# Performance work log

Measured on AMD Instinct MI355X. Metric: run time of the kernel, lower is better.

## Reference

```python
import jax, jax.numpy as jnp
import numpy as np

FEAT_STRIDE = 16
SCALES = np.array([8.0, 16.0, 32.0], np.float32)
RATIOS = np.array([0.5, 1.0, 2.0], np.float32)
PRE_NMS = 6000
POST_NMS = 300
NMS_THRESH = 0.7
MIN_SIZE = 16.0


def _base_anchors():
    bs = float(FEAT_STRIDE)
    ctr = (bs - 1.0) * 0.5
    size = bs * bs
    ws = np.round(np.sqrt(size / RATIOS))
    hs = np.round(ws * RATIOS)
    anchors = []
    for w, h in zip(ws, hs):
        for s in SCALES:
            ww, hh = w * s, h * s
            anchors.append([ctr - 0.5 * (ww - 1), ctr - 0.5 * (hh - 1),
                            ctr + 0.5 * (ww - 1), ctr + 0.5 * (hh - 1)])
    return np.array(anchors, np.float32)  # [A=9, 4]


def _all_anchors(H, W):
    base = _base_anchors()
    sx = np.arange(W, dtype=np.float32) * FEAT_STRIDE
    sy = np.arange(H, dtype=np.float32) * FEAT_STRIDE
    gx, gy = np.meshgrid(sx, sy)  # [H, W]
    shifts = np.stack([gx.ravel(), gy.ravel(), gx.ravel(), gy.ravel()], axis=1)  # [H*W, 4]
    return jnp.asarray((shifts[:, None, :] + base[None, :, :]).reshape(-1, 4))  # [H*W*A, 4]


def _conv2d(x, w, b, pad):
    y = jax.lax.conv_general_dilated(x, w, (1, 1), pad,
                                     dimension_numbers=('NCHW', 'OIHW', 'NCHW'))
    return y + b[None, :, None, None]


def _decode(anchors, deltas):
    wa = anchors[:, 2] - anchors[:, 0] + 1.0
    ha = anchors[:, 3] - anchors[:, 1] + 1.0
    cxa = anchors[:, 0] + 0.5 * wa
    cya = anchors[:, 1] + 0.5 * ha
    cx = deltas[:, 0] * wa + cxa
    cy = deltas[:, 1] * ha + cya
    w = wa * jnp.exp(deltas[:, 2])
    h = ha * jnp.exp(deltas[:, 3])
    return jnp.stack([cx - 0.5 * w, cy - 0.5 * h, cx + 0.5 * w, cy + 0.5 * h], axis=1)


def _pairwise_iou(b):
    x1, y1, x2, y2 = b[:, 0], b[:, 1], b[:, 2], b[:, 3]
    areas = (x2 - x1 + 1.0) * (y2 - y1 + 1.0)
    iw = jnp.clip(jnp.minimum(x2[:, None], x2[None, :]) - jnp.maximum(x1[:, None], x1[None, :]) + 1.0, 0.0)
    ih = jnp.clip(jnp.minimum(y2[:, None], y2[None, :]) - jnp.maximum(y1[:, None], y1[None, :]) + 1.0, 0.0)
    inter = iw * ih
    return inter / (areas[:, None] + areas[None, :] - inter)


def _proposal(bbox_pred, scores, anchors, im_info):
    boxes = _decode(anchors, bbox_pred)
    x1 = jnp.clip(boxes[:, 0], 0.0, im_info[1] - 1.0)
    y1 = jnp.clip(boxes[:, 1], 0.0, im_info[0] - 1.0)
    x2 = jnp.clip(boxes[:, 2], 0.0, im_info[1] - 1.0)
    y2 = jnp.clip(boxes[:, 3], 0.0, im_info[0] - 1.0)
    boxes = jnp.stack([x1, y1, x2, y2], axis=1)
    min_sz = MIN_SIZE * im_info[2]
    valid = ((x2 - x1 + 1.0) >= min_sz) & ((y2 - y1 + 1.0) >= min_sz)
    sc = jnp.where(valid, scores, -1.0)
    top_sc, idx = jax.lax.top_k(sc, PRE_NMS)
    props = boxes[idx]  # [PRE_NMS, 4], score-descending
    iou = _pairwise_iou(props)

    def body(i, keep):
        sup = (iou[i] > NMS_THRESH) & keep[i]
        return keep & ~(sup & (jnp.arange(PRE_NMS) > i))

    keep = jax.lax.fori_loop(0, PRE_NMS, body, jnp.ones((PRE_NMS,), bool))
    keep = keep & (top_sc > 0.0)
    order = jnp.argsort(jnp.logical_not(keep), stable=True)  # kept first, score order preserved
    sel = order[:POST_NMS]
    mask = (jnp.arange(POST_NMS) < jnp.sum(keep))[:, None]
    return jnp.where(mask, props[sel], 0.0)


def setup_inputs() -> dict:
    key = jax.random.key(0)
    ks = jax.random.split(key, 4)
    feature_map = jax.random.normal(ks[0], (1, 1024, 84, 125), jnp.float32)
    im_info = jnp.array([1344.0, 2000.0, 1.0], jnp.float32)  # (H, W, scale)
    conv_w = jax.random.normal(ks[1], (512, 1024, 3, 3), jnp.float32) * 0.01
    conv_b = jnp.zeros((512,), jnp.float32)
    cls_w = jax.random.normal(ks[2], (18, 512, 1, 1), jnp.float32) * 0.01
    cls_b = jnp.zeros((18,), jnp.float32)
    reg_w = jax.random.normal(ks[3], (36, 512, 1, 1), jnp.float32) * 0.01
    reg_b = jnp.zeros((36,), jnp.float32)
    return {"feature_map": feature_map, "im_info": im_info, "conv_w": conv_w,
            "conv_b": conv_b, "cls_w": cls_w, "cls_b": cls_b, "reg_w": reg_w, "reg_b": reg_b}


def reference(feature_map, im_info, conv_w, conv_b, cls_w, cls_b, reg_w, reg_b):
    B, C, H, W = feature_map.shape
    anchors = _all_anchors(H, W)  # [H*W*9, 4]
    fm = jax.nn.relu(_conv2d(feature_map, conv_w, conv_b, [(1, 1), (1, 1)]))
    cls = _conv2d(fm, cls_w, cls_b, [(0, 0), (0, 0)])  # [B, 18, H, W]
    reg = _conv2d(fm, reg_w, reg_b, [(0, 0), (0, 0)])  # [B, 36, H, W]
    cls_scores = cls.transpose(0, 2, 3, 1).reshape(-1, 2)
    bbox_pred = reg.transpose(0, 2, 3, 1).reshape(-1, 4)
    fg_probs = jax.nn.softmax(jax.lax.stop_gradient(cls_scores), axis=1)[:, 1]
    rois = _proposal(bbox_pred, fg_probs, anchors, im_info)
    return (bbox_pred, cls_scores, rois, anchors)
```

## Files before the change

kernel.cpp:

```cpp
#include <hip/hip_runtime.h>

typedef unsigned int u32;
typedef unsigned long long u64;

#define H_ 84
#define W_ 125
#define CIN 1024
#define CMID 512
#define NPOS 10500
#define NA 94500
#define PRE 6000
#define POST 300
#define FMROW 128
#define FMSTRIDE 10752
#define SELCAP 16384

__constant__ float c_aw[9] = {184.f, 368.f, 736.f, 128.f, 256.f, 512.f, 88.f, 176.f, 352.f};
__constant__ float c_ah[9] = { 96.f, 192.f, 384.f, 128.f, 256.f, 512.f, 176.f, 352.f, 704.f};

#define OFF_FM      0ull
#define OFF_BOXES   22020096ull
#define OFF_KEYS    23532096ull
#define OFF_SELA    24288096ull
#define OFF_SELB    24419168ull
#define OFF_PROPS   24550240ull
#define OFF_AREAS   24646240ull
#define OFF_VALIDW  24670240ull
#define OFF_MASK    24671008ull
#define OFF_KEEPW   29279008ull

__global__ __launch_bounds__(256, 4) void k_conv3(const float* __restrict__ in,
                                                  const float* __restrict__ w,
                                                  const float* __restrict__ bias,
                                                  float* __restrict__ fm) {
  __shared__ float Xs[16 * 4 * 132];
  const int tid = threadIdx.x;
  const int lane = tid & 63;
  const int wvi = __builtin_amdgcn_readfirstlane(tid >> 6);
  const int ocb = blockIdx.x;
  const int y0 = blockIdx.y * 2;
  const int oc0 = ocb * 16 + wvi * 4;

  float acc[4][2][2];
#pragma unroll
  for (int o = 0; o < 4; ++o)
#pragma unroll
    for (int r = 0; r < 2; ++r) {
      acc[o][r][0] = 0.f;
      acc[o][r][1] = 0.f;
    }

  const int cb = 2 * lane;

  float rbuf[33];
#pragma unroll
  for (int k = 0; k < 33; ++k) {
    const int l = tid + k * 256;
    const int r132 = l / 132;
    const int c = l - r132 * 132;
    const int i = r132 >> 2;
    const int rr = r132 & 3;
    const int yi = y0 - 1 + rr;
    const int xi = c - 1;
    float v = 0.f;
    if ((unsigned)yi < 84u && (unsigned)xi < 125u)
      v = in[i * (H_ * W_) + yi * W_ + xi];
    rbuf[k] = v;
  }

#pragma unroll 1
  for (int icb = 0; icb < CIN; icb += 16) {
    __syncthreads();
#pragma unroll
    for (int k = 0; k < 33; ++k) Xs[tid + k * 256] = rbuf[k];
    __syncthreads();

    const int icb2 = (icb + 16 < CIN) ? icb + 16 : icb;
#pragma unroll
    for (int k = 0; k < 33; ++k) {
      const int l = tid + k * 256;
      const int r132 = l / 132;
      const int c = l - r132 * 132;
      const int i = r132 >> 2;
      const int rr = r132 & 3;
      const int yi = y0 - 1 + rr;
      const int xi = c - 1;
      float v = 0.f;
      if ((unsigned)yi < 84u && (unsigned)xi < 125u)
        v = in[(icb2 + i) * (H_ * W_) + yi * W_ + xi];
      rbuf[k] = v;
    }

#pragma unroll 2
    for (int i = 0; i < 16; ++i) {
      const int ic = icb + i;
      float ws[4][9];
#pragma unroll
      for (int o = 0; o < 4; ++o)
#pragma unroll
        for (int e = 0; e < 9; ++e)
          ws[o][e] = w[(oc0 + o) * 9216 + ic * 9 + e];

      float x4[4][4];
#pragma unroll
      for (int rr = 0; rr < 4; ++rr) {
        float2 lo = *(const float2*)&Xs[(i * 4 + rr) * 132 + cb];
        float2 hi = *(const float2*)&Xs[(i * 4 + rr) * 132 + cb + 2];
        x4[rr][0] = lo.x;
        x4[rr][1] = lo.y;
        x4[rr][2] = hi.x;
        x4[rr][3] = hi.y;
      }

#pragma unroll
      for (int o = 0; o < 4; ++o)
#pragma unroll
        for (int r = 0; r < 2; ++r)
#pragma unroll
          for (int ky = 0; ky < 3; ++ky)
#pragma unroll
            for (int kx = 0; kx < 3; ++kx) {
              float wv2 = ws[o][ky * 3 + kx];
              acc[o][r][0] += wv2 * x4[r + ky][kx];
              acc[o][r][1] += wv2 * x4[r + ky][kx + 1];
            }
    }
  }

  const int px = 2 * lane;
#pragma unroll
  for (int o = 0; o < 4; ++o) {
    float b = bias[oc0 + o];
#pragma unroll
    for (int r = 0; r < 2; ++r) {
      float2 v;
      v.x = fmaxf(acc[o][r][0] + b, 0.f);
      v.y = fmaxf(acc[o][r][1] + b, 0.f);
      *(float2*)&fm[(oc0 + o) * FMSTRIDE + (y0 + r) * FMROW + px] = v;
    }
  }
}

__global__ __launch_bounds__(64) void k_heads(const float* __restrict__ fm,
                                              const float* __restrict__ cls_w,
                                              const float* __restrict__ cls_b,
                                              const float* __restrict__ reg_w,
                                              const float* __restrict__ reg_b,
                                              const float* __restrict__ iminfo,
                                              float* __restrict__ out_bbox,
                                              float* __restrict__ out_cls,
                                              float* __restrict__ out_anch,
                                              float* __restrict__ boxes,
                                              uint2* __restrict__ keys) {
  __shared__ float wl[64 * 56];
  const int tid = threadIdx.x;
  const int p = blockIdx.x * 64 + tid;
  const int pc = p < NPOS ? p : NPOS - 1;
  const int py = pc / W_;
  const int px = pc % W_;
  const int pos = py * FMROW + px;

  float acc[56];
#pragma unroll
  for (int o = 0; o < 56; ++o) acc[o] = 0.f;

#pragma unroll 1
  for (int icb = 0; icb < CMID; icb += 64) {
    __syncthreads();
    for (int l = tid; l < 64 * 54; l += 64) {
      int ic = l / 54;
      int o = l % 54;
      float wv = (o < 18) ? cls_w[o * CMID + icb + ic] : reg_w[(o - 18) * CMID + icb + ic];
      wl[ic * 56 + o] = wv;
    }
    __syncthreads();
#pragma unroll 4
    for (int i = 0; i < 64; ++i) {
      float v = fm[(icb + i) * FMSTRIDE + pos];
#pragma unroll
      for (int o4 = 0; o4 < 14; ++o4) {
        float4 w4 = *(const float4*)&wl[i * 56 + o4 * 4];
        acc[o4 * 4 + 0] += w4.x * v;
        acc[o4 * 4 + 1] += w4.y * v;
        acc[o4 * 4 + 2] += w4.z * v;
        acc[o4 * 4 + 3] += w4.w * v;
      }
    }
  }
  if (p >= NPOS) return;

  const float imh = iminfo[0];
  const float imw = iminfo[1];
  const float minsz = 16.0f * iminfo[2];

#pragma unroll
  for (int a = 0; a < 9; ++a) {
    const int n = p * 9 + a;
    float s0 = acc[a * 2 + 0] + cls_b[a * 2 + 0];
    float s1 = acc[a * 2 + 1] + cls_b[a * 2 + 1];
    out_cls[n * 2 + 0] = s0;
    out_cls[n * 2 + 1] = s1;

    float dx = acc[18 + a * 4 + 0] + reg_b[a * 4 + 0];
    float dy = acc[18 + a * 4 + 1] + reg_b[a * 4 + 1];
    float dw = acc[18 + a * 4 + 2] + reg_b[a * 4 + 2];
    float dh = acc[18 + a * 4 + 3] + reg_b[a * 4 + 3];
    out_bbox[n * 4 + 0] = dx;
    out_bbox[n * 4 + 1] = dy;
    out_bbox[n * 4 + 2] = dw;
    out_bbox[n * 4 + 3] = dh;

    float aw = c_aw[a], ah = c_ah[a];
    float cxs = px * 16.0f + 7.5f;
    float cys = py * 16.0f + 7.5f;
    float ax1 = cxs - 0.5f * (aw - 1.0f);
    float ay1 = cys - 0.5f * (ah - 1.0f);
    float ax2 = cxs + 0.5f * (aw - 1.0f);
    float ay2 = cys + 0.5f * (ah - 1.0f);
    out_anch[n * 4 + 0] = ax1;
    out_anch[n * 4 + 1] = ay1;
    out_anch[n * 4 + 2] = ax2;
    out_anch[n * 4 + 3] = ay2;

    float wa = ax2 - ax1 + 1.0f;
    float ha = ay2 - ay1 + 1.0f;
    float cxa = ax1 + 0.5f * wa;
    float cya = ay1 + 0.5f * ha;
    float cx = dx * wa + cxa;
    float cy = dy * ha + cya;
    float ww = wa * expf(dw);
    float hh = ha * expf(dh);
    float bx1 = cx - 0.5f * ww;
    float by1 = cy - 0.5f * hh;
    float bx2 = cx + 0.5f * ww;
    float by2 = cy + 0.5f * hh;
    bx1 = fminf(fmaxf(bx1, 0.f), imw - 1.f);
    by1 = fminf(fmaxf(by1, 0.f), imh - 1.f);
    bx2 = fminf(fmaxf(bx2, 0.f), imw - 1.f);
    by2 = fminf(fmaxf(by2, 0.f), imh - 1.f);
    boxes[n * 4 + 0] = bx1;
    boxes[n * 4 + 1] = by1;
    boxes[n * 4 + 2] = bx2;
    boxes[n * 4 + 3] = by2;

    bool valid = (bx2 - bx1 + 1.0f >= minsz) && (by2 - by1 + 1.0f >= minsz);
    float prob = 1.0f / (1.0f + expf(s0 - s1));
    u32 key = valid ? __float_as_uint(prob) : 0u;
    keys[n] = make_uint2(~key, (u32)n);
  }
}

__global__ __launch_bounds__(512) void k_select(const uint2* __restrict__ keys,
                                                uint2* __restrict__ selA,
                                                uint2* __restrict__ selB) {
  __shared__ u32 h[8192];
  __shared__ u32 stot[512];
  __shared__ u32 sB1, sLt1, sB2, sN;
  const int t = threadIdx.x;
  const int s = t * 185;
  const int e = (s + 185 < NA) ? s + 185 : NA;

  for (int i = t; i < 4096; i += 512) h[i] = 0;
  __syncthreads();
  for (int i = s; i < e; ++i) atomicAdd(&h[keys[i].x >> 20], 1u);
  __syncthreads();
  {
    u32 loc = 0;
#pragma unroll
    for (int j = 0; j < 8; ++j) loc += h[t * 8 + j];
    stot[t] = loc;
    __syncthreads();
    for (int off = 1; off < 512; off <<= 1) {
      u32 add = (t >= off) ? stot[t - off] : 0u;
      __syncthreads();
      stot[t] += add;
      __syncthreads();
    }
    u32 cb = stot[t] - loc;
    if (cb < PRE && stot[t] >= PRE) {
      u32 run = cb;
#pragma unroll
      for (int j = 0; j < 8; ++j) {
        u32 c = h[t * 8 + j];
        if (run < PRE && run + c >= PRE) { sB1 = t * 8 + j; sLt1 = run; }
        run += c;
      }
    }
  }
  __syncthreads();
  const u32 B1 = sB1;
  const u32 T2 = PRE - sLt1;

  for (int i = t; i < 4096; i += 512) h[i] = 0;
  __syncthreads();
  for (int i = s; i < e; ++i) {
    u32 k = keys[i].x;
    if ((k >> 20) == B1) atomicAdd(&h[(k >> 8) & 0xFFFu], 1u);
  }
  __syncthreads();
  {
    u32 loc = 0;
#pragma unroll
    for (int j = 0; j < 8; ++j) loc += h[t * 8 + j];
    stot[t] = loc;
    __syncthreads();
    for (int off = 1; off < 512; off <<= 1) {
      u32 add = (t >= off) ? stot[t - off] : 0u;
      __syncthreads();
      stot[t] += add;
      __syncthreads();
    }
    u32 cb = stot[t] - loc;
    if (cb < T2 && stot[t] >= T2) {
      u32 run = cb;
#pragma unroll
      for (int j = 0; j < 8; ++j) {
        u32 c = h[t * 8 + j];
        if (run < T2 && run + c >= T2) { sB2 = t * 8 + j; }
        run += c;
      }
    }
  }
  __syncthreads();
  const u32 B2 = sB2;

  u32 cnt = 0;
  for (int i = s; i < e; ++i) {
    u32 k = keys[i].x;
    u32 hi = k >> 20;
    if (hi < B1 || (hi == B1 && ((k >> 8) & 0xFFFu) <= B2)) cnt++;
  }
  stot[t] = cnt;
  __syncthreads();
  for (int off = 1; off < 512; off <<= 1) {
    u32 add = (t >= off) ? stot[t - off] : 0u;
    __syncthreads();
    stot[t] += add;
    __syncthreads();
  }
  u32 base = stot[t] - cnt;
  if (t == 511) sN = stot[511] < SELCAP ? stot[511] : SELCAP;
  for (int i = s; i < e; ++i) {
    uint2 v = keys[i];
    u32 hi = v.x >> 20;
    if (hi < B1 || (hi == B1 && ((v.x >> 8) & 0xFFFu) <= B2)) {
      if (base < SELCAP) selA[base] = v;
      base++;
    }
  }
  __syncthreads();
  const int n = (int)sN;

  const int q = (n + 511) / 512;
  const int s2 = t * q;
  const int e2 = (s2 + q < n) ? s2 + q : n;
  uint2* src = selA;
  uint2* dst = selB;
#pragma unroll 1
  for (int pass = 0; pass < 8; ++pass) {
    const int sh = pass * 4;
#pragma unroll
    for (int k = 0; k < 16; ++k) h[k * 512 + t] = 0;
    __syncthreads();
    for (int i = s2; i < e2; ++i) {
      u32 d = (src[i].x >> sh) & 15u;
      h[d * 512 + t] += 1;
    }
    __syncthreads();
    u32 run = 0;
#pragma unroll
    for (int j = 0; j < 16; ++j) {
      u32 v = h[t * 16 + j];
      h[t * 16 + j] = run;
      run += v;
    }
    stot[t] = run;
    __syncthreads();
    for (int off = 1; off < 512; off <<= 1) {
      u32 add = (t >= off) ? stot[t - off] : 0u;
      __syncthreads();
      stot[t] += add;
      __syncthreads();
    }
    u32 cb = (t > 0) ? stot[t - 1] : 0u;
#pragma unroll
    for (int j = 0; j < 16; ++j) h[t * 16 + j] += cb;
    __syncthreads();
    for (int i = s2; i < e2; ++i) {
      uint2 v = src[i];
      u32 d = (v.x >> sh) & 15u;
      u32 off = h[d * 512 + t];
      h[d * 512 + t] = off + 1;
      dst[off] = v;
    }
    __syncthreads();
    uint2* tmp = src;
    src = dst;
    dst = tmp;
  }
}

__global__ __launch_bounds__(256) void k_gather(const uint2* __restrict__ sel,
                                                const float4* __restrict__ boxes,
                                                float4* __restrict__ props,
                                                float* __restrict__ areas,
                                                u64* __restrict__ validw) {
  const int k = blockIdx.x * 256 + threadIdx.x;
  bool valid = false;
  if (k < PRE) {
    uint2 kv = sel[k];
    u32 key = ~kv.x;
    valid = key > 0u;
    float4 b = boxes[kv.y];
    props[k] = b;
    areas[k] = (b.z - b.x + 1.0f) * (b.w - b.y + 1.0f);
  }
  u64 bal = __ballot(valid);
  if ((threadIdx.x & 63) == 0 && k < PRE) validw[k >> 6] = bal;
}

__global__ __launch_bounds__(256) void k_iou(const float4* __restrict__ props,
                                             const float* __restrict__ areas,
                                             u64* __restrict__ mask) {
  __shared__ float4 pj[64];
  __shared__ float aj[64];
  const int t = threadIdx.x;
  const int jw = blockIdx.x;
  const int i = blockIdx.y * 256 + t;
  if (t < 64) {
    const int jj = jw * 64 + t;
    float4 z = {0.f, 0.f, 0.f, 0.f};
    pj[t] = (jj < PRE) ? props[jj] : z;
    aj[t] = (jj < PRE) ? areas[jj] : 0.f;
  }
  __syncthreads();
  if (i >= PRE) return;
  const int j0 = jw * 64;
  u64 bits = 0;
  if (j0 + 63 > i) {
    const float4 bi = props[i];
    const float ai = areas[i];
#pragma unroll 8
    for (int b = 0; b < 64; ++b) {
      const int j = j0 + b;
      if (j > i && j < PRE) {
        float4 bj = pj[b];
        float iw = fminf(bi.z, bj.z) - fmaxf(bi.x, bj.x) + 1.0f;
        float ih = fminf(bi.w, bj.w) - fmaxf(bi.y, bj.y) + 1.0f;
        iw = fmaxf(iw, 0.f);
        ih = fmaxf(ih, 0.f);
        float inter = iw * ih;
        if (inter > 0.7f * (ai + aj[b] - inter)) bits |= (1ull << b);
      }
    }
  }
  mask[(u64)i * 96 + jw] = bits;
}

__device__ __forceinline__ u64 bcast_u64(u64 v, int src) {
  u32 lo = (u32)v;
  u32 hi = (u32)(v >> 32);
  lo = (u32)__shfl((int)lo, src, 64);
  hi = (u32)__shfl((int)hi, src, 64);
  return ((u64)hi << 32) | (u64)lo;
}

__global__ __launch_bounds__(64) void k_nms(const u64* __restrict__ mask,
                                            const u64* __restrict__ validw,
                                            u64* __restrict__ keepw) {
  const int lane = threadIdx.x;
  const int w0 = (2 * lane < 96) ? 2 * lane : 0;
  const int w1 = (2 * lane < 96) ? 2 * lane + 1 : 1;
  u64 s0 = 0, s1 = 0;
  u64 b0[16], b1[16];
#pragma unroll
  for (int d = 0; d < 16; ++d) {
    b0[d] = mask[(u64)d * 96 + w0];
    b1[d] = mask[(u64)d * 96 + w1];
  }
#pragma unroll 1
  for (int i0 = 0; i0 < PRE; i0 += 16) {
#pragma unroll
    for (int d = 0; d < 16; ++d) {
      int i = i0 + d;
      int w = i >> 6;
      u64 cand = (w & 1) ? s1 : s0;
      u64 word = bcast_u64(cand, w >> 1);
      bool sup = (word >> (i & 63)) & 1ull;
      if (!sup) {
        s0 |= b0[d];
        s1 |= b1[d];
      }
      int ip = i + 16;
      if (ip > PRE - 1) ip = PRE - 1;
      b0[d] = mask[(u64)ip * 96 + w0];
      b1[d] = mask[(u64)ip * 96 + w1];
    }
  }
  if (2 * lane < 94) keepw[2 * lane] = ~s0 & validw[2 * lane];
  if (2 * lane + 1 < 94) keepw[2 * lane + 1] = ~s1 & validw[2 * lane + 1];
}

__global__ __launch_bounds__(128) void k_emit(const u64* __restrict__ keepw,
                                              const float4* __restrict__ props,
                                              float* __restrict__ rois) {
  __shared__ u32 base[94];
  const int t = threadIdx.x;
  for (int r = t; r < POST * 4; r += 128) rois[r] = 0.f;
  if (t < 94) base[t] = (u32)__popcll(keepw[t]);
  __syncthreads();
  if (t == 0) {
    u32 run = 0;
    for (int q = 0; q < 94; ++q) {
      u32 c = base[q];
      base[q] = run;
      run += c;
    }
  }
  __syncthreads();
  if (t < 94) {
    u64 kw = keepw[t];
    int rank = (int)base[t];
    while (kw) {
      int b = __ffsll((unsigned long long)kw) - 1;
      kw &= kw - 1;
      if (rank < POST) {
        float4 v = props[t * 64 + b];
        rois[rank * 4 + 0] = v.x;
        rois[rank * 4 + 1] = v.y;
        rois[rank * 4 + 2] = v.z;
        rois[rank * 4 + 3] = v.w;
      }
      rank++;
    }
  }
}

extern "C" void kernel_launch(void* const* d_in, const int* in_sizes, int n_in,
                              void* d_out, int out_size, void* d_ws, size_t ws_size,
                              hipStream_t stream) {
  const float* feat   = (const float*)d_in[0];
  const float* iminfo = (const float*)d_in[1];
  const float* conv_w = (const float*)d_in[2];
  const float* conv_b = (const float*)d_in[3];
  const float* cls_w  = (const float*)d_in[4];
  const float* cls_b  = (const float*)d_in[5];
  const float* reg_w  = (const float*)d_in[6];
  const float* reg_b  = (const float*)d_in[7];

  float* out = (float*)d_out;
  float* out_bbox = out;
  float* out_cls  = out + 378000;
  float* out_rois = out + 567000;
  float* out_anch = out + 568200;

  char* ws = (char*)d_ws;
  float* fm      = (float*)(ws + OFF_FM);
  float* boxes   = (float*)(ws + OFF_BOXES);
  uint2* keysA   = (uint2*)(ws + OFF_KEYS);
  uint2* selA    = (uint2*)(ws + OFF_SELA);
  uint2* selB    = (uint2*)(ws + OFF_SELB);
  float4* props  = (float4*)(ws + OFF_PROPS);
  float* areas   = (float*)(ws + OFF_AREAS);
  u64* validw    = (u64*)(ws + OFF_VALIDW);
  u64* mask      = (u64*)(ws + OFF_MASK);
  u64* keepw     = (u64*)(ws + OFF_KEEPW);

  k_conv3<<<dim3(32, 42), 256, 0, stream>>>(feat, conv_w, conv_b, fm);
  k_heads<<<165, 64, 0, stream>>>(fm, cls_w, cls_b, reg_w, reg_b, iminfo,
                                  out_bbox, out_cls, out_anch, boxes, keysA);
  k_select<<<1, 512, 0, stream>>>(keysA, selA, selB);
  k_gather<<<24, 256, 0, stream>>>(selA, (const float4*)boxes, props, areas, validw);
  k_iou<<<dim3(94, 24), 256, 0, stream>>>(props, areas, mask);
  k_nms<<<1, 64, 0, stream>>>(mask, validw, keepw);
  k_emit<<<1, 128, 0, stream>>>(keepw, props, out_rois);
}
```

Measured before the change: 3.261 ms.

## Double-buffer conv3 input tiles, swizzle block order, aggregate histogram atomics

The 3x3 conv kernel now uses two shared-memory buffers of 8 input channels each and precomputes gather offsets with a validity bitmask. This removes the per-iteration address arithmetic and one of the two barriers per step, and halves the register prefetch buffer. The launch becomes 1D with a swizzle that groups blocks sharing output rows, aiming for better L2 reuse of input rows. The select kernel's histogram passes now use wave-level ballot aggregation, so each distinct bin gets one shared atomic per wave instead of one per thread, at the cost of extra ballot and shuffle loops.

```diff
diff --git a/kernel.cpp b/kernel.cpp
--- a/kernel.cpp
+++ b/kernel.cpp
@@ -33,12 +33,14 @@
                                                   const float* __restrict__ w,
                                                   const float* __restrict__ bias,
                                                   float* __restrict__ fm) {
-  __shared__ float Xs[16 * 4 * 132];
+  __shared__ float Xs[2][8 * 4 * 132];
   const int tid = threadIdx.x;
   const int lane = tid & 63;
   const int wvi = __builtin_amdgcn_readfirstlane(tid >> 6);
-  const int ocb = blockIdx.x;
-  const int y0 = blockIdx.y * 2;
+  const int bid = blockIdx.x;
+  const int swz = (bid & 7) * 168 + (bid >> 3);
+  const int ocb = swz & 31;
+  const int y0 = (swz >> 5) * 2;
   const int oc0 = ocb * 16 + wvi * 4;
 
   float acc[4][2][2];
@@ -52,9 +54,10 @@
 
   const int cb = 2 * lane;
 
-  float rbuf[33];
-#pragma unroll
-  for (int k = 0; k < 33; ++k) {
+  u32 offk[17];
+  u32 vmask = 0;
+#pragma unroll
+  for (int k = 0; k < 17; ++k) {
     const int l = tid + k * 256;
     const int r132 = l / 132;
     const int c = l - r132 * 132;
@@ -62,37 +65,33 @@
     const int rr = r132 & 3;
     const int yi = y0 - 1 + rr;
     const int xi = c - 1;
-    float v = 0.f;
-    if ((unsigned)yi < 84u && (unsigned)xi < 125u)
-      v = in[i * (H_ * W_) + yi * W_ + xi];
-    rbuf[k] = v;
-  }
+    const bool ok = (l < 4224) && ((unsigned)yi < 84u) && ((unsigned)xi < 125u);
+    offk[k] = ok ? (u32)(i * (H_ * W_) + yi * W_ + xi) : 0u;
+    if (ok) vmask |= (1u << k);
+  }
+
+  float rb[17];
+#pragma unroll
+  for (int k = 0; k < 17; ++k) rb[k] = (vmask >> k & 1) ? in[offk[k]] : 0.f;
+#pragma unroll
+  for (int k = 0; k < 17; ++k) {
+    const int l = tid + k * 256;
+    if (l < 4224) Xs[0][l] = rb[k];
+  }
+  __syncthreads();
 
 #pragma unroll 1
-  for (int icb = 0; icb < CIN; icb += 16) {
-    __syncthreads();
-#pragma unroll
-    for (int k = 0; k < 33; ++k) Xs[tid + k * 256] = rbuf[k];
-    __syncthreads();
-
-    const int icb2 = (icb + 16 < CIN) ? icb + 16 : icb;
-#pragma unroll
-    for (int k = 0; k < 33; ++k) {
-      const int l = tid + k * 256;
-      const int r132 = l / 132;
-      const int c = l - r132 * 132;
-      const int i = r132 >> 2;
-      const int rr = r132 & 3;
-      const int yi = y0 - 1 + rr;
-      const int xi = c - 1;
-      float v = 0.f;
-      if ((unsigned)yi < 84u && (unsigned)xi < 125u)
-        v = in[(icb2 + i) * (H_ * W_) + yi * W_ + xi];
-      rbuf[k] = v;
-    }
-
+  for (int t = 0; t < 128; ++t) {
+    const int cur = t & 1;
+    const int icn = (t + 1 < 128) ? (t + 1) * 8 : t * 8;
+    const u32 gbase = (u32)icn * (u32)(H_ * W_);
+#pragma unroll
+    for (int k = 0; k < 17; ++k)
+      rb[k] = (vmask >> k & 1) ? in[gbase + offk[k]] : 0.f;
+
+    const int icb = t * 8;
 #pragma unroll 2
-    for (int i = 0; i < 16; ++i) {
+    for (int i = 0; i < 8; ++i) {
       const int ic = icb + i;
       float ws[4][9];
 #pragma unroll
@@ -104,8 +103,8 @@
       float x4[4][4];
 #pragma unroll
       for (int rr = 0; rr < 4; ++rr) {
-        float2 lo = *(const float2*)&Xs[(i * 4 + rr) * 132 + cb];
-        float2 hi = *(const float2*)&Xs[(i * 4 + rr) * 132 + cb + 2];
+        float2 lo = *(const float2*)&Xs[cur][(i * 4 + rr) * 132 + cb];
+        float2 hi = *(const float2*)&Xs[cur][(i * 4 + rr) * 132 + cb + 2];
         x4[rr][0] = lo.x;
         x4[rr][1] = lo.y;
         x4[rr][2] = hi.x;
@@ -120,17 +119,24 @@
           for (int ky = 0; ky < 3; ++ky)
 #pragma unroll
             for (int kx = 0; kx < 3; ++kx) {
-              float wv2 = ws[o][ky * 3 + kx];
+              const float wv2 = ws[o][ky * 3 + kx];
               acc[o][r][0] += wv2 * x4[r + ky][kx];
               acc[o][r][1] += wv2 * x4[r + ky][kx + 1];
             }
     }
+
+#pragma unroll
+    for (int k = 0; k < 17; ++k) {
+      const int l = tid + k * 256;
+      if (l < 4224) Xs[cur ^ 1][l] = rb[k];
+    }
+    __syncthreads();
   }
 
   const int px = 2 * lane;
 #pragma unroll
   for (int o = 0; o < 4; ++o) {
-    float b = bias[oc0 + o];
+    const float b = bias[oc0 + o];
 #pragma unroll
     for (int r = 0; r < 2; ++r) {
       float2 v;
@@ -257,12 +263,25 @@
   __shared__ u32 stot[512];
   __shared__ u32 sB1, sLt1, sB2, sN;
   const int t = threadIdx.x;
+  const int lane = t & 63;
   const int s = t * 185;
   const int e = (s + 185 < NA) ? s + 185 : NA;
 
   for (int i = t; i < 4096; i += 512) h[i] = 0;
   __syncthreads();
-  for (int i = s; i < e; ++i) atomicAdd(&h[keys[i].x >> 20], 1u);
+  for (int k0 = 0; k0 < 185; ++k0) {
+    const int i = s + k0;
+    bool act = i < e;
+    u32 bin = act ? (keys[i].x >> 20) : 0u;
+    while (__any(act)) {
+      u64 am = __ballot(act);
+      int leader = (int)(__ffsll((unsigned long long)am) - 1);
+      u32 lb = (u32)__shfl((int)bin, leader, 64);
+      u64 same = __ballot(act && bin == lb);
+      if (lane == leader) atomicAdd(&h[lb], (u32)__popcll(same));
+      if (act && bin == lb) act = false;
+    }
+  }
   __syncthreads();
   {
     u32 loc = 0;
@@ -293,9 +312,19 @@
 
   for (int i = t; i < 4096; i += 512) h[i] = 0;
   __syncthreads();
-  for (int i = s; i < e; ++i) {
-    u32 k = keys[i].x;
-    if ((k >> 20) == B1) atomicAdd(&h[(k >> 8) & 0xFFFu], 1u);
+  for (int k0 = 0; k0 < 185; ++k0) {
+    const int i = s + k0;
+    u32 kx = (i < e) ? keys[i].x : 0u;
+    bool act = (i < e) && ((kx >> 20) == B1);
+    u32 bin = (kx >> 8) & 0xFFFu;
+    while (__any(act)) {
+      u64 am = __ballot(act);
+      int leader = (int)(__ffsll((unsigned long long)am) - 1);
+      u32 lb = (u32)__shfl((int)bin, leader, 64);
+      u64 same = __ballot(act && bin == lb);
+      if (lane == leader && same) atomicAdd(&h[lb], (u32)__popcll(same));
+      if (act && bin == lb) act = false;
+    }
   }
   __syncthreads();
   {
@@ -566,7 +595,7 @@
   u64* mask      = (u64*)(ws + OFF_MASK);
   u64* keepw     = (u64*)(ws + OFF_KEEPW);
 
-  k_conv3<<<dim3(32, 42), 256, 0, stream>>>(feat, conv_w, conv_b, fm);
+  k_conv3<<<1344, 256, 0, stream>>>(feat, conv_w, conv_b, fm);
   k_heads<<<165, 64, 0, stream>>>(fm, cls_w, cls_b, reg_w, reg_b, iminfo,
                                   out_bbox, out_cls, out_anch, boxes, keysA);
   k_select<<<1, 512, 0, stream>>>(keysA, selA, selB);
```

New measurement: 3.380 ms. 1.04x slower.

## Use packed FP32 FMA in conv3x3 and remap blocks across XCDs

Applied to the files above, without the earlier changes.

Rewrites the 3x3 conv inner loop to use v_pk_fma_f32 through inline asm, with weights packed into scalar register pairs, so each instruction does two FMAs. It also flattens the grid to 1D and remaps block ids so each XCD works on a contiguous group of output-channel blocks, aiming for better L2 reuse of weights. The input prefetch now precomputes offsets and a validity mask once instead of recomputing index math every iteration. The risks are inline asm constraints (an SGPR operand needs uniform weights) and higher register pressure.

```diff
diff --git a/kernel.cpp b/kernel.cpp
--- a/kernel.cpp
+++ b/kernel.cpp
@@ -15,6 +15,11 @@
 #define FMSTRIDE 10752
 #define SELCAP 16384
 
+#define PK_FMA_LO(a, x, w64) \
+  asm("v_pk_fma_f32 %0, %1, %2, %0 op_sel_hi:[1,0,1]" : "+v"(a) : "v"(x), "s"(w64))
+#define PK_FMA_HI(a, x, w64) \
+  asm("v_pk_fma_f32 %0, %1, %2, %0 op_sel:[0,1,0] op_sel_hi:[1,1,1]" : "+v"(a) : "v"(x), "s"(w64))
+
 __constant__ float c_aw[9] = {184.f, 368.f, 736.f, 128.f, 256.f, 512.f, 88.f, 176.f, 352.f};
 __constant__ float c_ah[9] = { 96.f, 192.f, 384.f, 128.f, 256.f, 512.f, 176.f, 352.f, 704.f};
 
@@ -37,22 +42,23 @@
   const int tid = threadIdx.x;
   const int lane = tid & 63;
   const int wvi = __builtin_amdgcn_readfirstlane(tid >> 6);
-  const int ocb = blockIdx.x;
-  const int y0 = blockIdx.y * 2;
+  const int bid = blockIdx.x;
+  const int xcd = bid & 7;
+  const int r = bid >> 3;
+  const int ocb = xcd * 4 + (r & 3);
+  const int y0 = (r >> 2) * 2;
   const int oc0 = ocb * 16 + wvi * 4;
 
-  float acc[4][2][2];
+  float2 acc2[4][2];
 #pragma unroll
   for (int o = 0; o < 4; ++o)
 #pragma unroll
-    for (int r = 0; r < 2; ++r) {
-      acc[o][r][0] = 0.f;
-      acc[o][r][1] = 0.f;
-    }
+    for (int rr = 0; rr < 2; ++rr) acc2[o][rr] = make_float2(0.f, 0.f);
 
   const int cb = 2 * lane;
 
-  float rbuf[33];
+  u32 offk[33];
+  u64 vmask = 0;
 #pragma unroll
   for (int k = 0; k < 33; ++k) {
     const int l = tid + k * 256;
@@ -62,81 +68,79 @@
     const int rr = r132 & 3;
     const int yi = y0 - 1 + rr;
     const int xi = c - 1;
-    float v = 0.f;
-    if ((unsigned)yi < 84u && (unsigned)xi < 125u)
-      v = in[i * (H_ * W_) + yi * W_ + xi];
-    rbuf[k] = v;
-  }
+    const bool ok = ((unsigned)yi < 84u) && ((unsigned)xi < 125u);
+    offk[k] = ok ? (u32)(i * (H_ * W_) + yi * W_ + xi) : 0u;
+    if (ok) vmask |= (1ull << k);
+  }
+
+  float rb[33];
+#pragma unroll
+  for (int k = 0; k < 33; ++k) rb[k] = (vmask >> k & 1) ? in[offk[k]] : 0.f;
 
 #pragma unroll 1
   for (int icb = 0; icb < CIN; icb += 16) {
     __syncthreads();
 #pragma unroll
-    for (int k = 0; k < 33; ++k) Xs[tid + k * 256] = rbuf[k];
-    __syncthreads();
-
-    const int icb2 = (icb + 16 < CIN) ? icb + 16 : icb;
-#pragma unroll
-    for (int k = 0; k < 33; ++k) {
-      const int l = tid + k * 256;
-      const int r132 = l / 132;
-      const int c = l - r132 * 132;
-      const int i = r132 >> 2;
-      const int rr = r132 & 3;
-      const int yi = y0 - 1 + rr;
-      const int xi = c - 1;
-      float v = 0.f;
-      if ((unsigned)yi < 84u && (unsigned)xi < 125u)
-        v = in[(icb2 + i) * (H_ * W_) + yi * W_ + xi];
-      rbuf[k] = v;
-    }
+    for (int k = 0; k < 33; ++k) Xs[tid + k * 256] = rb[k];
+    __syncthreads();
+
+    const u32 gbase = (u32)((icb + 16 < CIN) ? icb + 16 : icb) * (u32)(H_ * W_);
+#pragma unroll
+    for (int k = 0; k < 33; ++k)
+      rb[k] = (vmask >> k & 1) ? in[gbase + offk[k]] : 0.f;
 
 #pragma unroll 2
     for (int i = 0; i < 16; ++i) {
       const int ic = icb + i;
-      float ws[4][9];
-#pragma unroll
-      for (int o = 0; o < 4; ++o)
-#pragma unroll
-        for (int e = 0; e < 9; ++e)
-          ws[o][e] = w[(oc0 + o) * 9216 + ic * 9 + e];
-
-      float x4[4][4];
+
+      float2 P[4][3];
 #pragma unroll
       for (int rr = 0; rr < 4; ++rr) {
         float2 lo = *(const float2*)&Xs[(i * 4 + rr) * 132 + cb];
         float2 hi = *(const float2*)&Xs[(i * 4 + rr) * 132 + cb + 2];
-        x4[rr][0] = lo.x;
-        x4[rr][1] = lo.y;
-        x4[rr][2] = hi.x;
-        x4[rr][3] = hi.y;
-      }
-
-#pragma unroll
-      for (int o = 0; o < 4; ++o)
-#pragma unroll
-        for (int r = 0; r < 2; ++r)
-#pragma unroll
-          for (int ky = 0; ky < 3; ++ky)
-#pragma unroll
-            for (int kx = 0; kx < 3; ++kx) {
-              float wv2 = ws[o][ky * 3 + kx];
-              acc[o][r][0] += wv2 * x4[r + ky][kx];
-              acc[o][r][1] += wv2 * x4[r + ky][kx + 1];
-            }
+        P[rr][0] = lo;
+        P[rr][1] = make_float2(lo.y, hi.x);
+        P[rr][2] = hi;
+      }
+
+#pragma unroll
+      for (int o = 0; o < 4; ++o) {
+        const float* wrow = &w[(oc0 + o) * 9216 + ic * 9];
+        float wf[9];
+#pragma unroll
+        for (int e = 0; e < 9; ++e) wf[e] = wrow[e];
+        u64 wp[4];
+#pragma unroll
+        for (int q = 0; q < 4; ++q)
+          wp[q] = ((u64)__float_as_uint(wf[2 * q + 1]) << 32) |
+                  (u64)__float_as_uint(wf[2 * q]);
+#pragma unroll
+        for (int rr = 0; rr < 2; ++rr) {
+          PK_FMA_LO(acc2[o][rr], P[rr + 0][0], wp[0]);
+          PK_FMA_HI(acc2[o][rr], P[rr + 0][1], wp[0]);
+          PK_FMA_LO(acc2[o][rr], P[rr + 0][2], wp[1]);
+          PK_FMA_HI(acc2[o][rr], P[rr + 1][0], wp[1]);
+          PK_FMA_LO(acc2[o][rr], P[rr + 1][1], wp[2]);
+          PK_FMA_HI(acc2[o][rr], P[rr + 1][2], wp[2]);
+          PK_FMA_LO(acc2[o][rr], P[rr + 2][0], wp[3]);
+          PK_FMA_HI(acc2[o][rr], P[rr + 2][1], wp[3]);
+          acc2[o][rr].x += wf[8] * P[rr + 2][2].x;
+          acc2[o][rr].y += wf[8] * P[rr + 2][2].y;
+        }
+      }
     }
   }
 
   const int px = 2 * lane;
 #pragma unroll
   for (int o = 0; o < 4; ++o) {
-    float b = bias[oc0 + o];
-#pragma unroll
-    for (int r = 0; r < 2; ++r) {
+    const float b = bias[oc0 + o];
+#pragma unroll
+    for (int rr = 0; rr < 2; ++rr) {
       float2 v;
-      v.x = fmaxf(acc[o][r][0] + b, 0.f);
-      v.y = fmaxf(acc[o][r][1] + b, 0.f);
-      *(float2*)&fm[(oc0 + o) * FMSTRIDE + (y0 + r) * FMROW + px] = v;
+      v.x = fmaxf(acc2[o][rr].x + b, 0.f);
+      v.y = fmaxf(acc2[o][rr].y + b, 0.f);
+      *(float2*)&fm[(oc0 + o) * FMSTRIDE + (y0 + rr) * FMROW + px] = v;
     }
   }
 }
@@ -566,7 +570,7 @@
   u64* mask      = (u64*)(ws + OFF_MASK);
   u64* keepw     = (u64*)(ws + OFF_KEEPW);
 
-  k_conv3<<<dim3(32, 42), 256, 0, stream>>>(feat, conv_w, conv_b, fm);
+  k_conv3<<<1344, 256, 0, stream>>>(feat, conv_w, conv_b, fm);
   k_heads<<<165, 64, 0, stream>>>(fm, cls_w, cls_b, reg_w, reg_b, iminfo,
                                   out_bbox, out_cls, out_anch, boxes, keysA);
   k_select<<<1, 512, 0, stream>>>(keysA, selA, selB);
```

Result: faster. 3.168 ms (-2.8%).
